# Performance work log

Measured on AMD Instinct MI355X. Metric: run time of the kernel, lower is better.

Reference implementation:

```python
import jax, jax.numpy as jnp
import numpy as np

B = 262144
MA = [128, 128]
MB = [128, 128]


def krone_linear(x_a, x_b, wa, wb, ba, bb):
    # slice inputs to each branch's in_features (torch slices the wider branch)
    ia, ib = wa.shape[1], wb.shape[1]
    x_a = x_a[:, :ia]
    x_b = x_b[:, :ib]
    h_a = x_a @ wa.T + ba
    h_b = x_b @ wb.T + bb
    # zero-pad the narrower output so both branches share a width (static shapes)
    oa, ob = wa.shape[0], wb.shape[0]
    if oa > ob:
        h_b = jnp.pad(h_b, ((0, 0), (0, oa - ob)))
    elif ob > oa:
        h_a = jnp.pad(h_a, ((0, 0), (0, ob - oa)))
    return h_a, h_b


def krone_softmax(x_a, x_b, fa, fb):
    x_a = x_a[:, :fa]
    x_b = x_b[:, :fb]
    # vectorized per-row Kronecker product: kron(a, b)[i*fb + j] = a[i]*b[j]
    y = (x_a[:, :, None] * x_b[:, None, :]).reshape(x_a.shape[0], fa * fb)
    return jax.nn.softmax(y, axis=1)


def setup_inputs() -> dict:
    key = jax.random.key(0)
    ks = jax.random.split(key, 13)
    s = 0.1
    inp = {
        "x": jax.random.normal(ks[0], (2, B, 2), dtype=jnp.float32),
        "w1a": jax.random.normal(ks[1], (MA[0], 2), dtype=jnp.float32) * s,
        "w1b": jax.random.normal(ks[2], (MB[0], 2), dtype=jnp.float32) * s,
        "b1a": jax.random.normal(ks[3], (MA[0],), dtype=jnp.float32) * s,
        "b1b": jax.random.normal(ks[4], (MB[0],), dtype=jnp.float32) * s,
        "w2a": jax.random.normal(ks[5], (MA[1], MA[0]), dtype=jnp.float32) * s,
        "w2b": jax.random.normal(ks[6], (MB[1], MB[0]), dtype=jnp.float32) * s,
        "b2a": jax.random.normal(ks[7], (MA[1],), dtype=jnp.float32) * s,
        "b2b": jax.random.normal(ks[8], (MB[1],), dtype=jnp.float32) * s,
        "w3a": jax.random.normal(ks[9], (1, MA[1]), dtype=jnp.float32) * s,
        "w3b": jax.random.normal(ks[10], (3, MB[1]), dtype=jnp.float32) * s,
        "b3a": jax.random.normal(ks[11], (1,), dtype=jnp.float32) * s,
        "b3b": jax.random.normal(ks[12], (3,), dtype=jnp.float32) * s,
    }
    return inp


def reference(x, w1a, w1b, b1a, b1b, w2a, w2b, b2a, b2b, w3a, w3b, b3a, b3b):
    x_a, x_b = x[0], x[1]
    h_a, h_b = krone_linear(x_a, x_b, w1a, w1b, b1a, b1b)
    h_a, h_b = jax.nn.relu(h_a), jax.nn.relu(h_b)
    h_a, h_b = krone_linear(h_a, h_b, w2a, w2b, b2a, b2b)
    h_a, h_b = jax.nn.relu(h_a), jax.nn.relu(h_b)
    h_a, h_b = krone_linear(h_a, h_b, w3a, w3b, b3a, b3b)
    return krone_softmax(h_a, h_b, 1, 3)
```

## Files before the change

### kernel.cpp

```cpp
#include <hip/hip_runtime.h>
#include <hip/hip_bf16.h>


#define BTOT 262144
#define NBLK (BTOT / 256)

typedef __attribute__((ext_vector_type(4))) float floatx4;
typedef __attribute__((ext_vector_type(8))) short bf16x8;
typedef __attribute__((ext_vector_type(4))) int  intx4;

#define OFF_W2  0
#define OFF_W1  32768
#define OFF_B2  35072
#define OFF_W3  35584

static __device__ __forceinline__ int pack2bf(float lo, float hi) {
    unsigned a = __builtin_bit_cast(unsigned, lo) + 0x8000u;
    unsigned b = __builtin_bit_cast(unsigned, hi) + 0x8000u;
    return (int)__builtin_amdgcn_perm(b, a, 0x07060302u);
}

#define SEL4(a0, a1, a2, a3, i) \
    ((i) == 0 ? (a0) : (i) == 1 ? (a1) : (i) == 2 ? (a2) : (a3))

static __device__ __forceinline__ float redcol(float v) {
    v += __shfl_xor(v, 1); v += __shfl_xor(v, 2);
    v += __shfl_xor(v, 4); v += __shfl_xor(v, 8);
    return v;
}

static __device__ __forceinline__ int w1slot(int k) { return k + (k >> 3); }

static __device__ __forceinline__ void pack_path(
        unsigned char* smem, int tid,
        const float* __restrict__ w2, const float* __restrict__ w1,
        const float* __restrict__ b1, const float* __restrict__ b2) {
    const float4* w2p = (const float4*)w2;
    #pragma unroll
    for (int i = 0; i < 16; ++i) {
        int u = i * 256 + tid;
        int n = u >> 5;
        float4 f = w2p[u];
        int k = (u & 31) * 4;
        int s = k >> 5;
        int j0 = k & 7;
        int l = ((k & 31) >> 3) * 16 + (n & 15);
        int2 pkd;
        pkd.x = pack2bf(f.x, f.y);
        pkd.y = pack2bf(f.z, f.w);
        *(int2*)(smem + OFF_W2 + (s * 8 + (n >> 4)) * 1024 + l * 16 + j0 * 2) = pkd;
    }
    if (tid < 128) {
        ((float4*)(smem + OFF_W1))[w1slot(tid)] =
            make_float4(w1[2 * tid], w1[2 * tid + 1], b1[tid], 0.f);
        ((float*)(smem + OFF_B2))[tid] = b2[tid];
    }
}

#define GEMM_CHUNK(acc, xv, W1p, W2p, B2p)                                     \
    {                                                                          \
        _Pragma("unroll")                                                      \
        for (int t = 0; t < 8; ++t) {                                          \
            float b2n = (B2p)[t * 16 + col];                                   \
            floatx4 bi = (floatx4){b2n, b2n, b2n, b2n};                        \
            _Pragma("unroll")                                                  \
            for (int mt = 0; mt < 2; ++mt) acc[t][mt] = bi;                    \
        }                                                                      \
        _Pragma("unroll")                                                      \
        for (int s = 0; s < 4; ++s) {                                          \
            intx4 af[2];                                                       \
            const int bslot = s * 36 + quad * 9;                               \
            _Pragma("unroll")                                                  \
            for (int j2 = 0; j2 < 4; ++j2) {                                   \
                float4 c0 = (W1p)[bslot + 2 * j2];                             \
                float4 c1 = (W1p)[bslot + 2 * j2 + 1];                         \
                _Pragma("unroll")                                              \
                for (int mt = 0; mt < 2; ++mt) {                               \
                    float h0 = fmaxf(fmaf(xv[mt].x, c0.x,                      \
                                fmaf(xv[mt].y, c0.y, c0.z)), 0.f);             \
                    float h1 = fmaxf(fmaf(xv[mt].x, c1.x,                      \
                                fmaf(xv[mt].y, c1.y, c1.z)), 0.f);             \
                    af[mt][j2] = pack2bf(h0, h1);                              \
                }                                                              \
            }                                                                  \
            _Pragma("unroll")                                                  \
            for (int t = 0; t < 8; ++t) {                                      \
                bf16x8 bfr = (W2p)[(s * 8 + t) * 64 + lane];                   \
                _Pragma("unroll")                                              \
                for (int mt = 0; mt < 2; ++mt)                                 \
                    acc[t][mt] = __builtin_amdgcn_mfma_f32_16x16x32_bf16(      \
                        __builtin_bit_cast(bf16x8, af[mt]), bfr,               \
                        acc[t][mt], 0, 0, 0);                                  \
            }                                                                  \
        }                                                                      \
    }

__global__ __launch_bounds__(256, 2)
void krone_a(const float* __restrict__ x,
             const float* __restrict__ w1a, const float* __restrict__ b1a,
             const float* __restrict__ w2a, const float* __restrict__ b2a,
             const float* __restrict__ w3a, const float* __restrict__ b3a,
             float* __restrict__ sa_out) {
    __shared__ __align__(16) unsigned char smem[36096];
    const int tid = threadIdx.x;
    pack_path(smem, tid, w2a, w1a, b1a, b2a);
    if (tid < 128) ((float*)(smem + OFF_W3))[tid] = w3a[tid];
    __syncthreads();

    const int lane = tid & 63;
    const int wave = tid >> 6;
    const int quad = lane >> 4;
    const int col  = lane & 15;
    const bf16x8* W2 = (const bf16x8*)(smem + OFF_W2);
    const float4* W1 = (const float4*)(smem + OFF_W1);
    const float*  B2 = (const float*)(smem + OFF_B2);
    const float*  W3 = (const float*)(smem + OFF_W3);
    const float2* xp = (const float2*)x;
    const float b3 = b3a[0];

    #pragma unroll
    for (int c = 0; c < 2; ++c) {
        __builtin_amdgcn_sched_barrier(0);
        const int base = blockIdx.x * 256 + c * 128 + wave * 32;
        float2 xv[2];
        #pragma unroll
        for (int mt = 0; mt < 2; ++mt) xv[mt] = xp[base + mt * 16 + col];

        floatx4 acc[8][2];
        GEMM_CHUNK(acc, xv, W1, W2, B2);
        __builtin_amdgcn_sched_barrier(0);

        float pa[2][4] = {};
        #pragma unroll
        for (int t = 0; t < 8; ++t) {
            float w3n = W3[t * 16 + col];
            #pragma unroll
            for (int mt = 0; mt < 2; ++mt)
                #pragma unroll
                for (int r = 0; r < 4; ++r)
                    pa[mt][r] = fmaf(w3n, fmaxf(acc[t][mt][r], 0.f), pa[mt][r]);
        }
        #pragma unroll
        for (int mt = 0; mt < 2; ++mt)
            #pragma unroll
            for (int r = 0; r < 4; ++r) pa[mt][r] = redcol(pa[mt][r]);
        __builtin_amdgcn_sched_barrier(0);

        if (col < 4) {
            #pragma unroll
            for (int mt = 0; mt < 2; ++mt) {
                int sl = mt * 16 + quad * 4 + col;
                sa_out[base + sl] =
                    SEL4(pa[mt][0], pa[mt][1], pa[mt][2], pa[mt][3], col) + b3;
            }
        }
        __builtin_amdgcn_sched_barrier(0);
    }
}

__global__ __launch_bounds__(256, 2)
void krone_b(const float* __restrict__ x,
             const float* __restrict__ w1b, const float* __restrict__ b1b,
             const float* __restrict__ w2b, const float* __restrict__ b2b,
             const float* __restrict__ w3b, const float* __restrict__ b3b,
             const float* __restrict__ sa_in, float* __restrict__ out) {
    __shared__ __align__(16) unsigned char smem[37120];
    const int tid = threadIdx.x;
    pack_path(smem, tid, w2b, w1b, b1b, b2b);
    for (int i = tid; i < 384; i += 256) ((float*)(smem + OFF_W3))[i] = w3b[i];
    __syncthreads();

    const int lane = tid & 63;
    const int wave = tid >> 6;
    const int quad = lane >> 4;
    const int col  = lane & 15;
    const bf16x8* W2 = (const bf16x8*)(smem + OFF_W2);
    const float4* W1 = (const float4*)(smem + OFF_W1);
    const float*  B2 = (const float*)(smem + OFF_B2);
    const float*  W3 = (const float*)(smem + OFF_W3);
    const float2* xp = (const float2*)x + BTOT;
    const float b30 = b3b[0], b31 = b3b[1], b32 = b3b[2];

    #pragma unroll
    for (int c = 0; c < 2; ++c) {
        __builtin_amdgcn_sched_barrier(0);
        const int base = blockIdx.x * 256 + c * 128 + wave * 32;
        float2 xv[2];
        #pragma unroll
        for (int mt = 0; mt < 2; ++mt) xv[mt] = xp[base + mt * 16 + col];

        floatx4 acc[8][2];
        GEMM_CHUNK(acc, xv, W1, W2, B2);
        __builtin_amdgcn_sched_barrier(0);

        float p0[2][4] = {}, p1[2][4] = {}, p2[2][4] = {};
        #pragma unroll
        for (int t = 0; t < 8; ++t) {
            int n = t * 16 + col;
            float w30 = W3[n], w31 = W3[128 + n], w32 = W3[256 + n];
            #pragma unroll
            for (int mt = 0; mt < 2; ++mt)
                #pragma unroll
                for (int r = 0; r < 4; ++r) {
                    float h = fmaxf(acc[t][mt][r], 0.f);
                    p0[mt][r] = fmaf(w30, h, p0[mt][r]);
                    p1[mt][r] = fmaf(w31, h, p1[mt][r]);
                    p2[mt][r] = fmaf(w32, h, p2[mt][r]);
                }
        }
        #pragma unroll
        for (int mt = 0; mt < 2; ++mt)
            #pragma unroll
            for (int r = 0; r < 4; ++r) {
                p0[mt][r] = redcol(p0[mt][r]);
                p1[mt][r] = redcol(p1[mt][r]);
                p2[mt][r] = redcol(p2[mt][r]);
            }
        __builtin_amdgcn_sched_barrier(0);

        if (col < 4) {
            #pragma unroll
            for (int mt = 0; mt < 2; ++mt) {
                int sl = mt * 16 + quad * 4 + col;
                float t0 = SEL4(p0[mt][0], p0[mt][1], p0[mt][2], p0[mt][3], col) + b30;
                float t1 = SEL4(p1[mt][0], p1[mt][1], p1[mt][2], p1[mt][3], col) + b31;
                float t2 = SEL4(p2[mt][0], p2[mt][1], p2[mt][2], p2[mt][3], col) + b32;
                float sa = sa_in[base + sl];
                float y0 = sa * t0, y1 = sa * t1, y2 = sa * t2;
                float m = fmaxf(y0, fmaxf(y1, y2));
                float e0 = __expf(y0 - m), e1 = __expf(y1 - m), e2 = __expf(y2 - m);
                float rs = 1.f / (e0 + e1 + e2);
                long o = (long)(base + sl) * 3;
                out[o]     = e0 * rs;
                out[o + 1] = e1 * rs;
                out[o + 2] = e2 * rs;
            }
        }
        __builtin_amdgcn_sched_barrier(0);
    }
}

extern "C" void kernel_launch(void* const* d_in, const int* in_sizes, int n_in,
                              void* d_out, int out_size, void* d_ws, size_t ws_size,
                              hipStream_t stream) {
    const float* x   = (const float*)d_in[0];
    const float* w1a = (const float*)d_in[1];
    const float* w1b = (const float*)d_in[2];
    const float* b1a = (const float*)d_in[3];
    const float* b1b = (const float*)d_in[4];
    const float* w2a = (const float*)d_in[5];
    const float* w2b = (const float*)d_in[6];
    const float* b2a = (const float*)d_in[7];
    const float* b2b = (const float*)d_in[8];
    const float* w3a = (const float*)d_in[9];
    const float* w3b = (const float*)d_in[10];
    const float* b3a = (const float*)d_in[11];
    const float* b3b = (const float*)d_in[12];
    float* sa = (float*)d_ws;
    float* out = (float*)d_out;

    krone_a<<<NBLK, 256, 0, stream>>>(x, w1a, b1a, w2a, b2a, w3a, b3a, sa);
    krone_b<<<NBLK, 256, 0, stream>>>(x, w1b, b1b, w2b, b2b, w3b, b3b, sa, out);
}
```

Baseline: 119.3 us.

## Fuse branch A and B kernels into one, keep intermediate in LDS

Merges the two per-branch kernels into a single kernel that runs branch A, writes its scalar result to shared memory, repacks branch-B weights into the same LDS region, and then runs branch B with the softmax epilogue. It also preloads both branches' inputs up front. This removes one kernel launch and the global round-trip of the intermediate array. In exchange, each block must pack weights twice with an extra barrier, which serializes the weight setup within each block.

```diff
diff --git a/kernel.cpp b/kernel.cpp
--- a/kernel.cpp
+++ b/kernel.cpp
@@ -13,6 +13,8 @@
 #define OFF_W1  32768
 #define OFF_B2  35072
 #define OFF_W3  35584
+#define OFF_SA  37120
+#define LDS_TOTAL 38144
 
 static __device__ __forceinline__ int pack2bf(float lo, float hi) {
     unsigned a = __builtin_bit_cast(unsigned, lo) + 0x8000u;
@@ -57,7 +59,7 @@
     }
 }
 
-#define GEMM_CHUNK(acc, xv, W1p, W2p, B2p)                                     \
+#define GEMM_CHUNK(acc, XV, W1p, W2p, B2p)                                     \
     {                                                                          \
         _Pragma("unroll")                                                      \
         for (int t = 0; t < 8; ++t) {                                          \
@@ -76,10 +78,10 @@
                 float4 c1 = (W1p)[bslot + 2 * j2 + 1];                         \
                 _Pragma("unroll")                                              \
                 for (int mt = 0; mt < 2; ++mt) {                               \
-                    float h0 = fmaxf(fmaf(xv[mt].x, c0.x,                      \
-                                fmaf(xv[mt].y, c0.y, c0.z)), 0.f);             \
-                    float h1 = fmaxf(fmaf(xv[mt].x, c1.x,                      \
-                                fmaf(xv[mt].y, c1.y, c1.z)), 0.f);             \
+                    float h0 = fmaxf(fmaf((XV)[mt].x, c0.x,                    \
+                                fmaf((XV)[mt].y, c0.y, c0.z)), 0.f);           \
+                    float h1 = fmaxf(fmaf((XV)[mt].x, c1.x,                    \
+                                fmaf((XV)[mt].y, c1.y, c1.z)), 0.f);           \
                     af[mt][j2] = pack2bf(h0, h1);                              \
                 }                                                              \
             }                                                                  \
@@ -96,38 +98,51 @@
     }
 
 __global__ __launch_bounds__(256, 2)
-void krone_a(const float* __restrict__ x,
-             const float* __restrict__ w1a, const float* __restrict__ b1a,
-             const float* __restrict__ w2a, const float* __restrict__ b2a,
-             const float* __restrict__ w3a, const float* __restrict__ b3a,
-             float* __restrict__ sa_out) {
-    __shared__ __align__(16) unsigned char smem[36096];
-    const int tid = threadIdx.x;
-    pack_path(smem, tid, w2a, w1a, b1a, b2a);
-    if (tid < 128) ((float*)(smem + OFF_W3))[tid] = w3a[tid];
-    __syncthreads();
-
+void krone_fused(const float* __restrict__ x,
+                 const float* __restrict__ w1a, const float* __restrict__ w1b,
+                 const float* __restrict__ b1a, const float* __restrict__ b1b,
+                 const float* __restrict__ w2a, const float* __restrict__ w2b,
+                 const float* __restrict__ b2a, const float* __restrict__ b2b,
+                 const float* __restrict__ w3a, const float* __restrict__ w3b,
+                 const float* __restrict__ b3a, const float* __restrict__ b3b,
+                 float* __restrict__ out) {
+    __shared__ __align__(16) unsigned char smem[LDS_TOTAL];
+
+    const int tid  = threadIdx.x;
     const int lane = tid & 63;
     const int wave = tid >> 6;
     const int quad = lane >> 4;
     const int col  = lane & 15;
+
+    const float2* xA = (const float2*)x;
+    const float2* xB = xA + BTOT;
+    float2 xa[4], xb[4];
+    #pragma unroll
+    for (int c = 0; c < 2; ++c)
+        #pragma unroll
+        for (int mt = 0; mt < 2; ++mt) {
+            int idx = blockIdx.x * 256 + c * 128 + wave * 32 + mt * 16 + col;
+            xa[c * 2 + mt] = xA[idx];
+            xb[c * 2 + mt] = xB[idx];
+        }
+    const float b3a_ = b3a[0];
+    const float b30 = b3b[0], b31 = b3b[1], b32 = b3b[2];
+
     const bf16x8* W2 = (const bf16x8*)(smem + OFF_W2);
     const float4* W1 = (const float4*)(smem + OFF_W1);
     const float*  B2 = (const float*)(smem + OFF_B2);
     const float*  W3 = (const float*)(smem + OFF_W3);
-    const float2* xp = (const float2*)x;
-    const float b3 = b3a[0];
+    float*        SA = (float*)(smem + OFF_SA);
+
+    pack_path(smem, tid, w2a, w1a, b1a, b2a);
+    if (tid < 128) ((float*)(smem + OFF_W3))[tid] = w3a[tid];
+    __syncthreads();
 
     #pragma unroll
     for (int c = 0; c < 2; ++c) {
         __builtin_amdgcn_sched_barrier(0);
-        const int base = blockIdx.x * 256 + c * 128 + wave * 32;
-        float2 xv[2];
-        #pragma unroll
-        for (int mt = 0; mt < 2; ++mt) xv[mt] = xp[base + mt * 16 + col];
-
         floatx4 acc[8][2];
-        GEMM_CHUNK(acc, xv, W1, W2, B2);
+        GEMM_CHUNK(acc, xa + 2 * c, W1, W2, B2);
         __builtin_amdgcn_sched_barrier(0);
 
         float pa[2][4] = {};
@@ -150,47 +165,23 @@
             #pragma unroll
             for (int mt = 0; mt < 2; ++mt) {
                 int sl = mt * 16 + quad * 4 + col;
-                sa_out[base + sl] =
-                    SEL4(pa[mt][0], pa[mt][1], pa[mt][2], pa[mt][3], col) + b3;
+                SA[c * 128 + wave * 32 + sl] =
+                    SEL4(pa[mt][0], pa[mt][1], pa[mt][2], pa[mt][3], col) + b3a_;
             }
         }
         __builtin_amdgcn_sched_barrier(0);
     }
-}
-
-__global__ __launch_bounds__(256, 2)
-void krone_b(const float* __restrict__ x,
-             const float* __restrict__ w1b, const float* __restrict__ b1b,
-             const float* __restrict__ w2b, const float* __restrict__ b2b,
-             const float* __restrict__ w3b, const float* __restrict__ b3b,
-             const float* __restrict__ sa_in, float* __restrict__ out) {
-    __shared__ __align__(16) unsigned char smem[37120];
-    const int tid = threadIdx.x;
+
+    __syncthreads();
     pack_path(smem, tid, w2b, w1b, b1b, b2b);
     for (int i = tid; i < 384; i += 256) ((float*)(smem + OFF_W3))[i] = w3b[i];
     __syncthreads();
 
-    const int lane = tid & 63;
-    const int wave = tid >> 6;
-    const int quad = lane >> 4;
-    const int col  = lane & 15;
-    const bf16x8* W2 = (const bf16x8*)(smem + OFF_W2);
-    const float4* W1 = (const float4*)(smem + OFF_W1);
-    const float*  B2 = (const float*)(smem + OFF_B2);
-    const float*  W3 = (const float*)(smem + OFF_W3);
-    const float2* xp = (const float2*)x + BTOT;
-    const float b30 = b3b[0], b31 = b3b[1], b32 = b3b[2];
-
     #pragma unroll
     for (int c = 0; c < 2; ++c) {
         __builtin_amdgcn_sched_barrier(0);
-        const int base = blockIdx.x * 256 + c * 128 + wave * 32;
-        float2 xv[2];
-        #pragma unroll
-        for (int mt = 0; mt < 2; ++mt) xv[mt] = xp[base + mt * 16 + col];
-
         floatx4 acc[8][2];
-        GEMM_CHUNK(acc, xv, W1, W2, B2);
+        GEMM_CHUNK(acc, xb + 2 * c, W1, W2, B2);
         __builtin_amdgcn_sched_barrier(0);
 
         float p0[2][4] = {}, p1[2][4] = {}, p2[2][4] = {};
@@ -225,12 +216,12 @@
                 float t0 = SEL4(p0[mt][0], p0[mt][1], p0[mt][2], p0[mt][3], col) + b30;
                 float t1 = SEL4(p1[mt][0], p1[mt][1], p1[mt][2], p1[mt][3], col) + b31;
                 float t2 = SEL4(p2[mt][0], p2[mt][1], p2[mt][2], p2[mt][3], col) + b32;
-                float sa = sa_in[base + sl];
+                float sa = SA[c * 128 + wave * 32 + sl];
                 float y0 = sa * t0, y1 = sa * t1, y2 = sa * t2;
                 float m = fmaxf(y0, fmaxf(y1, y2));
                 float e0 = __expf(y0 - m), e1 = __expf(y1 - m), e2 = __expf(y2 - m);
                 float rs = 1.f / (e0 + e1 + e2);
-                long o = (long)(base + sl) * 3;
+                long o = (long)(blockIdx.x * 256 + c * 128 + wave * 32 + sl) * 3;
                 out[o]     = e0 * rs;
                 out[o + 1] = e1 * rs;
                 out[o + 2] = e2 * rs;
@@ -256,9 +247,8 @@
     const float* w3b = (const float*)d_in[10];
     const float* b3a = (const float*)d_in[11];
     const float* b3b = (const float*)d_in[12];
-    float* sa = (float*)d_ws;
     float* out = (float*)d_out;
 
-    krone_a<<<NBLK, 256, 0, stream>>>(x, w1a, b1a, w2a, b2a, w3a, b3a, sa);
-    krone_b<<<NBLK, 256, 0, stream>>>(x, w1b, b1b, w2b, b2b, w3b, b3b, sa, out);
-}
+    krone_fused<<<NBLK, 256, 0, stream>>>(x, w1a, w1b, b1a, b1b, w2a, w2b,
+                                          b2a, b2b, w3a, w3b, b3a, b3b, out);
+}
```

Result: no change. 119.9 us (+0.5%).
